# Performance work log

Hardware: AMD Instinct MI355X
Metric: run time of the kernel (lower is better)

Reference implementation:

```python
import jax, jax.numpy as jnp
import numpy as np

B, N, C, H = 4, 1025, 768, 12
KEEP_RATIO = 0.25
BETA = 1.0


def setup_inputs() -> dict:
    key = jax.random.key(0)
    k1, k2, k3, k4, k5 = jax.random.split(key, 5)
    x = jax.random.normal(k1, (B, N, C), dtype=jnp.float32)
    ucb_count_score = jax.random.uniform(k2, (H, N), dtype=jnp.float32)
    W_qkv = jax.random.normal(k3, (C, 3 * C), dtype=jnp.float32) * 0.02
    W_proj = jax.random.normal(k4, (C, C), dtype=jnp.float32) * 0.02
    b_proj = jax.random.normal(k5, (C,), dtype=jnp.float32) * 0.02
    return {"x": x, "ucb_count_score": ucb_count_score, "W_qkv": W_qkv,
            "W_proj": W_proj, "b_proj": b_proj, "counter": 100, "ucb_enabled": 1}


def reference(x, ucb_count_score, W_qkv, W_proj, b_proj, counter, ucb_enabled):
    Bn, Nn, Cn = x.shape
    Dh = Cn // H
    scale = Dh ** -0.5
    # qkv projection (no bias, qkv_bias=False)
    qkv = (x @ W_qkv).reshape(Bn, Nn, 3, H, Dh)
    q = jnp.transpose(qkv[:, :, 0], (0, 2, 1, 3))  # [B,H,N,Dh]
    k = jnp.transpose(qkv[:, :, 1], (0, 2, 1, 3))
    v = jnp.transpose(qkv[:, :, 2], (0, 2, 1, 3))
    attn_probs = jax.nn.softmax(jnp.einsum('bhnd,bhmd->bhnm', q, k) * scale, axis=-1)

    if ucb_enabled and counter > 50:
        # UCB pruning path (exclude_cls=True, keep_ratio set)
        total_patches = Nn - 1
        k_sel = max(1, int(total_patches * KEEP_RATIO))
        patch_scores = attn_probs[:, :, :, 1:].mean(axis=2)  # [B,H,N-1]
        expl = BETA * jnp.sqrt(jnp.log(counter + 1.0) / (ucb_count_score[:, 1:] + 1e-6))  # [H,N-1]
        global_ucb = (patch_scores + expl[None]).mean(axis=1)  # [B,N-1]
        _, sel = jax.lax.top_k(global_ucb, k_sel)  # [B,k]
        tok = sel + 1  # shift for CLS
        # keep[b,j] = 1 if token j is CLS or selected in batch b
        keep = jnp.zeros((Bn, Nn), dtype=attn_probs.dtype)
        keep = keep.at[jnp.arange(Bn)[:, None], tok].set(1.0).at[:, 0].set(1.0)
        # mask[b,h,i,j] = keep[b,i] OR keep[b,j]
        mask = jnp.maximum(keep[:, None, :, None], keep[:, None, None, :])
        pruned = attn_probs * mask
        pruned = pruned / (pruned.sum(axis=-1, keepdims=True) + 1e-8)
        context = jnp.einsum('bhnm,bhmd->bhnd', pruned, v)
        cnt = jnp.zeros((Nn,), dtype=jnp.float32).at[tok.reshape(-1)].add(1.0) / Bn
        score_delta = jnp.broadcast_to(cnt[None, :], ucb_count_score.shape)
    else:
        context = jnp.einsum('bhnm,bhmd->bhnd', attn_probs, v)
        score_delta = None

    out = context.transpose(0, 2, 1, 3).reshape(Bn, Nn, Cn) @ W_proj + b_proj
    return out, score_delta
```

## Files before the change

kernel.cpp:

```cpp
#include <hip/hip_runtime.h>
#include <hip/hip_bf16.h>
#include <math.h>

#define Bb 4
#define Nn 1025
#define Cc 768
#define Hh 12
#define BH (Bb*Hh)
#define M_ROWS 4100
#define KSEL 256
#define JP 1152
#define IT_TILES 68
#define NIB 17
#define NIB32 33
#define NSW 9
#define MT16 264
#define KC24 24
#define JT16 72
#define STR4 292
#define NPART 396
#define QSCALE 0.18033688011112042f

#define CAST_X_BLK 1584
#define CAST_WQKV_BLK 864
#define CAST_WPROJ_BLK 288

typedef __attribute__((ext_vector_type(8))) short short8;
typedef __attribute__((ext_vector_type(4))) short short4s;
typedef __attribute__((ext_vector_type(4))) float floatx4;

static __device__ inline unsigned short f2bf(float v) {
    __hip_bfloat16 b = __float2bfloat16(v);
    return *reinterpret_cast<unsigned short*>(&b);
}
static __device__ inline short tbfs(float f) {
    union { float f; unsigned u; } x; x.f = f;
    return (short)(x.u >> 16);
}
static __device__ inline float fexp2(float x) {
    return __builtin_amdgcn_exp2f(x);
}

static __device__ inline void async16(const unsigned short* g, unsigned short* l) {
    __builtin_amdgcn_global_load_lds(
        (const __attribute__((address_space(1))) unsigned int*)g,
        (__attribute__((address_space(3))) unsigned int*)l, 16, 0, 0);
}

__global__ __launch_bounds__(256)
void cast_all(const float* __restrict__ x, const float* __restrict__ Wqkv,
              const float* __restrict__ Wproj,
              unsigned short* __restrict__ xA, unsigned short* __restrict__ WB,
              unsigned short* __restrict__ WpB)
{
    int blk = blockIdx.x;
    int tid = threadIdx.x;
    if (blk < CAST_X_BLK) {
        int s = blk * 256 + tid;
        int ml = s & 15, q = (s >> 4) & 3;
        int t2 = s >> 6;
        int mt = t2 % MT16, kc = t2 / MT16;
        int m = mt * 16 + ml, k = kc * 32 + q * 8;
        uint4 pk = {0u, 0u, 0u, 0u};
        if (m < M_ROWS) {
            float4 a = *(const float4*)&x[(size_t)m * 768 + k];
            float4 b2 = *(const float4*)&x[(size_t)m * 768 + k + 4];
            pk.x = (unsigned)f2bf(a.x)  | ((unsigned)f2bf(a.y)  << 16);
            pk.y = (unsigned)f2bf(a.z)  | ((unsigned)f2bf(a.w)  << 16);
            pk.z = (unsigned)f2bf(b2.x) | ((unsigned)f2bf(b2.y) << 16);
            pk.w = (unsigned)f2bf(b2.z) | ((unsigned)f2bf(b2.w) << 16);
        }
        *(uint4*)&xA[(size_t)s * 8] = pk;
        return;
    }
    const float* W;
    unsigned short* WO;
    int N, NT, s;
    if (blk < CAST_X_BLK + CAST_WQKV_BLK) {
        W = Wqkv; WO = WB; N = 2304; NT = 144;
        s = (blk - CAST_X_BLK) * 256 + tid;
    } else {
        W = Wproj; WO = WpB; N = 768; NT = 48;
        s = (blk - CAST_X_BLK - CAST_WQKV_BLK) * 256 + tid;
    }
    int nl = s & 15, q = (s >> 4) & 3;
    int t2 = s >> 6;
    int nt = t2 % NT, kc = t2 / NT;
    int n = nt * 16 + nl, k = kc * 32 + q * 8;
    unsigned hv[8];
#pragma unroll
    for (int e = 0; e < 8; ++e)
        hv[e] = f2bf(W[(size_t)(k + e) * N + n]);
    uint4 pk;
    pk.x = hv[0] | (hv[1] << 16);
    pk.y = hv[2] | (hv[3] << 16);
    pk.z = hv[4] | (hv[5] << 16);
    pk.w = hv[6] | (hv[7] << 16);
    *(uint4*)&WO[(size_t)s * 8] = pk;
}

__global__ __launch_bounds__(256, 2)
void gemm_mfma(const unsigned short* __restrict__ Af,
               const unsigned short* __restrict__ Bf,
               int Nt16, int mode,
               unsigned short* __restrict__ qB, unsigned short* __restrict__ kF,
               unsigned short* __restrict__ vF,
               float* __restrict__ outp, const float* __restrict__ bias)
{
    __shared__ __align__(16) unsigned short ldsA[4096];
    __shared__ __align__(16) unsigned short ldsB[4096];
    const int tid = threadIdx.x;
    const int ln = tid & 63, w = tid >> 6;
    const int wm = w >> 1, wn = w & 1;
    const int mb = blockIdx.x, nb = blockIdx.y;

    floatx4 acc[4][4];
#pragma unroll
    for (int mt = 0; mt < 4; ++mt)
#pragma unroll
        for (int nt = 0; nt < 4; ++nt)
            acc[mt][nt] = (floatx4){0.f, 0.f, 0.f, 0.f};

    for (int kc = 0; kc < KC24; ++kc) {
        const unsigned short* gA = Af + ((size_t)(kc * MT16 + mb * 8)) * 512;
        const unsigned short* gB = Bf + ((size_t)(kc * Nt16 + nb * 8)) * 512;
        async16(gA + (size_t)(w * 128 + ln) * 8,      &ldsA[w * 1024]);
        async16(gA + (size_t)(w * 128 + 64 + ln) * 8, &ldsA[w * 1024 + 512]);
        async16(gB + (size_t)(w * 128 + ln) * 8,      &ldsB[w * 1024]);
        async16(gB + (size_t)(w * 128 + 64 + ln) * 8, &ldsB[w * 1024 + 512]);
        __syncthreads();

        short8 Am[4], Bn[4];
#pragma unroll
        for (int mt = 0; mt < 4; ++mt)
            Am[mt] = *(const short8*)&ldsA[((wm * 4 + mt) * 64 + ln) * 8];
#pragma unroll
        for (int nt = 0; nt < 4; ++nt)
            Bn[nt] = *(const short8*)&ldsB[((wn * 4 + nt) * 64 + ln) * 8];
#pragma unroll
        for (int mt = 0; mt < 4; ++mt)
#pragma unroll
            for (int nt = 0; nt < 4; ++nt)
                acc[mt][nt] = __builtin_amdgcn_mfma_f32_16x16x32_bf16(
                    Am[mt], Bn[nt], acc[mt][nt], 0, 0, 0);
        __syncthreads();
    }

    const int q = ln >> 4, l15 = ln & 15;
    if (mode == 1) {
#pragma unroll
        for (int nt = 0; nt < 4; ++nt) {
            int gn = nb * 128 + wn * 64 + nt * 16 + l15;
            float bv = bias[gn];
#pragma unroll
            for (int mt = 0; mt < 4; ++mt) {
                int gmb = mb * 128 + wm * 64 + mt * 16 + q * 4;
#pragma unroll
                for (int r = 0; r < 4; ++r) {
                    int gm = gmb + r;
                    if (gm < M_ROWS)
                        outp[(size_t)gm * 768 + gn] = acc[mt][nt][r] + bv;
                }
            }
        }
    } else {
#pragma unroll
        for (int nt = 0; nt < 4; ++nt) {
            int gn = nb * 128 + wn * 64 + nt * 16 + l15;
            int s = (gn >= 1536) ? 2 : (gn >= 768 ? 1 : 0);
            int rr = gn - s * Cc;
            int h = rr >> 6, d = rr & 63;
#pragma unroll
            for (int mt = 0; mt < 4; ++mt) {
                int gmb = mb * 128 + wm * 64 + mt * 16 + q * 4;
#pragma unroll
                for (int r = 0; r < 4; ++r) {
                    int gm = gmb + r;
                    if (gm >= M_ROWS) continue;
                    int b = gm / Nn;
                    int n = gm - b * Nn;
                    int bh = b * Hh + h;
                    float val = acc[mt][nt][r];
                    if (s == 0) {
                        int idx = (((bh * IT_TILES + (n >> 4)) * 2 + (d >> 5)) * 512)
                                  + ((((d & 31) >> 3) * 16 + (n & 15)) * 8) + (d & 7);
                        qB[idx] = f2bf(val * QSCALE);
                    } else if (s == 1) {
                        size_t idx = ((((size_t)bh * JT16 + (n >> 4)) * 2 + (d >> 5)) * 64
                                      + ((d >> 3) & 3) * 16 + (n & 15)) * 8 + (d & 7);
                        kF[idx] = f2bf(val);
                    } else {
                        size_t idx = ((((size_t)bh * JT16 + (n >> 4)) * 4 + (d >> 4)) * 64
                                      + ((n >> 2) & 3) * 16 + (d & 15)) * 4 + (n & 3);
                        vF[idx] = f2bf(val);
                    }
                }
            }
        }
    }
}

__global__ __launch_bounds__(256, 4)
void attn_colsum_mfma(const unsigned short* __restrict__ qB,
                      const unsigned short* __restrict__ kF,
                      float* __restrict__ colsum_part)
{
    __shared__ unsigned int expS8[32 * STR4];
    __shared__ float red16[16][32];
    __shared__ float linv[32];

    const int blk = blockIdx.x;
    const int x8 = blk & 7, g = blk >> 3;
    const int bh = x8 * 6 + (g % 6);
    const int ib = g / 6;
    const int tid = threadIdx.x;
    const int ws = tid >> 6;
    const int ln = tid & 63;
    const int i16 = ln & 15, q = ln >> 4;

    const unsigned short* kBase = kF + (size_t)bh * JT16 * 1024;

    short8 Qf[2][2];
#pragma unroll
    for (int it = 0; it < 2; ++it)
#pragma unroll
        for (int kc = 0; kc < 2; ++kc)
            Qf[it][kc] = *(const short8*)&qB[(((size_t)bh * IT_TILES + ib * 2 + it) * 2 + kc) * 512 + ln * 8];

    float lacc[2][2] = {{0.f, 0.f}, {0.f, 0.f}};

    short8 Kc[2][2], Kn[2][2];
#pragma unroll
    for (int jt = 0; jt < 2; ++jt)
#pragma unroll
        for (int kc = 0; kc < 2; ++kc)
            Kc[jt][kc] = *(const short8*)&kBase[(((ws * 2 + jt) * 2 + kc) * 64 + ln) * 8];

    for (int sw = 0; sw < NSW; ++sw) {
        if (sw + 1 < NSW) {
#pragma unroll
            for (int jt = 0; jt < 2; ++jt)
#pragma unroll
                for (int kc = 0; kc < 2; ++kc)
                    Kn[jt][kc] = *(const short8*)&kBase[((((sw + 1) * 8 + ws * 2 + jt) * 2 + kc) * 64 + ln) * 8];
        }

        floatx4 S[2][2];
#pragma unroll
        for (int it = 0; it < 2; ++it)
#pragma unroll
            for (int jt = 0; jt < 2; ++jt) {
                S[it][jt] = (floatx4){0.f, 0.f, 0.f, 0.f};
#pragma unroll
                for (int kc = 0; kc < 2; ++kc)
                    S[it][jt] = __builtin_amdgcn_mfma_f32_16x16x32_bf16(Kc[jt][kc], Qf[it][kc], S[it][jt], 0, 0, 0);
            }

        const int jbase0 = sw * 128 + ws * 32 + q * 4;
#pragma unroll
        for (int it = 0; it < 2; ++it) {
            const int irow = it * 16 + i16;
#pragma unroll
            for (int jt = 0; jt < 2; ++jt) {
                int jbase = jbase0 + jt * 16;
                float p[4];
#pragma unroll
                for (int r = 0; r < 4; ++r) {
                    float vld = (jbase + r < Nn) ? 1.f : 0.f;
                    p[r] = fexp2(S[it][jt][r]) * vld;
                }
                lacc[it][jt] += (p[0] + p[1]) + (p[2] + p[3]);
                unsigned u = (unsigned)__builtin_amdgcn_cvt_pk_fp8_f32(p[0], p[1], 0, false);
                u = (unsigned)__builtin_amdgcn_cvt_pk_fp8_f32(p[2], p[3], (int)u, true);
                expS8[irow * STR4 + (jbase >> 2)] = u;
            }
        }
#pragma unroll
        for (int jt = 0; jt < 2; ++jt)
#pragma unroll
            for (int kc = 0; kc < 2; ++kc)
                Kc[jt][kc] = Kn[jt][kc];
    }

    __syncthreads();
#pragma unroll
    for (int it = 0; it < 2; ++it)
        red16[ws * 4 + q][it * 16 + i16] = lacc[it][0] + lacc[it][1];
    __syncthreads();
    if (tid < 32) {
        float s = 0.f;
#pragma unroll
        for (int t = 0; t < 16; ++t) s += red16[t][tid];
        int gi = ib * 32 + tid;
        linv[tid] = (gi < Nn) ? 1.f / s : 0.f;
    }
    __syncthreads();

    float* prow = colsum_part + (size_t)(bh * NIB32 + ib) * JP;
    for (int grp = tid; grp < 288; grp += 256) {
        float a0 = 0.f, a1 = 0.f, a2 = 0.f, a3 = 0.f;
#pragma unroll 8
        for (int i = 0; i < 32; ++i) {
            unsigned v = expS8[i * STR4 + grp];
            float li = linv[i];
            a0 += __builtin_amdgcn_cvt_f32_fp8(v, 0) * li;
            a1 += __builtin_amdgcn_cvt_f32_fp8(v, 1) * li;
            a2 += __builtin_amdgcn_cvt_f32_fp8(v, 2) * li;
            a3 += __builtin_amdgcn_cvt_f32_fp8(v, 3) * li;
        }
        float4 o = {a0, a1, a2, a3};
        *(float4*)&prow[grp * 4] = o;
    }
}

__global__ __launch_bounds__(1024)
void ucb_topk(const float* __restrict__ colsum_part, const float* __restrict__ ucb_score,
              const int* __restrict__ counter_p,
              float* __restrict__ keepP, float* __restrict__ cnt_b)
{
    const int b = blockIdx.x;
    const int tid = threadIdx.x;
    __shared__ float vals[1024];
    __shared__ int   idxs[1024];

    for (int t = tid; t < JP; t += 1024) {
        keepP[b * JP + t] = 0.f;
        cnt_b[b * JP + t] = 0.f;
    }

    const int j = tid + 1;
    const float* pb = colsum_part + (size_t)b * NPART * JP + j;
    float c0 = 0.f, c1 = 0.f, c2 = 0.f, c3 = 0.f;
#pragma unroll 4
    for (int g2 = 0; g2 < NPART; g2 += 4) {
        c0 += pb[(size_t)(g2 + 0) * JP];
        c1 += pb[(size_t)(g2 + 1) * JP];
        c2 += pb[(size_t)(g2 + 2) * JP];
        c3 += pb[(size_t)(g2 + 3) * JP];
    }
    float cs = (c0 + c1) + (c2 + c3);

    float lc = logf((float)(*counter_p) + 1.0f);
    float s = cs * (1.0f / (float)Nn);
#pragma unroll
    for (int h = 0; h < Hh; ++h)
        s += sqrtf(lc / (ucb_score[h * Nn + j] + 1e-6f));
    s *= (1.0f / (float)Hh);
    vals[tid] = s; idxs[tid] = tid;
    __syncthreads();

    for (int k = 2; k <= 1024; k <<= 1) {
        for (int jj = k >> 1; jj > 0; jj >>= 1) {
            int partner = tid ^ jj;
            if (partner > tid) {
                float v1 = vals[tid], v2 = vals[partner];
                int i1 = idxs[tid], i2 = idxs[partner];
                bool gt = (v1 > v2) || (v1 == v2 && i1 < i2);
                bool desc = ((tid & k) == 0);
                if (desc ? !gt : gt) {
                    vals[tid] = v2; vals[partner] = v1;
                    idxs[tid] = i2; idxs[partner] = i1;
                }
            }
            __syncthreads();
        }
    }

    if (tid < KSEL) {
        int tok = idxs[tid] + 1;
        keepP[b * JP + tok] = 1.f;
        cnt_b[b * JP + tok] = 1.0f / (float)Bb;
    }
    if (tid == 0) keepP[b * JP + 0] = 1.f;
}

__global__ __launch_bounds__(256, 2)
void attn_ctx_mfma(const unsigned short* __restrict__ qB,
                   const unsigned short* __restrict__ kF,
                   const unsigned short* __restrict__ vF,
                   const float* __restrict__ keepP, const float* __restrict__ cnt_b,
                   unsigned short* __restrict__ ctxA, float* __restrict__ out2)
{
    __shared__ __align__(16) char smem[25856];
    float* keeps = (float*)smem;
    float* red16 = (float*)(smem + 4608);
    float* dinv  = (float*)(smem + 8704);
    float* redC  = (float*)(smem + 8960);

    const int blk = blockIdx.x;
    const int x8 = blk & 7, g = blk >> 3;
    const int bh = x8 * 6 + (g % 6);
    const int ib = g / 6;
    const int b = bh / Hh, h = bh % Hh;
    const int tid = threadIdx.x;
    const int ws = tid >> 6;
    const int ln = tid & 63;
    const int i16 = ln & 15, q = ln >> 4;

    {
        int t = blk * 256 + tid;
        if (t < Hh * Nn) {
            int n = t % Nn;
            out2[t] = cnt_b[0 * JP + n] + cnt_b[1 * JP + n]
                    + cnt_b[2 * JP + n] + cnt_b[3 * JP + n];
        }
    }

    for (int t = tid; t < JP; t += 256) keeps[t] = keepP[b * JP + t];

    const unsigned short* kBase = kF + (size_t)bh * JT16 * 1024;
    const unsigned short* vBase = vF + (size_t)bh * JT16 * 1024;

    short8 Qf[4][2];
#pragma unroll
    for (int it = 0; it < 4; ++it)
#pragma unroll
        for (int kc = 0; kc < 2; ++kc)
            Qf[it][kc] = *(const short8*)&qB[(((size_t)bh * IT_TILES + ib * 4 + it) * 2 + kc) * 512 + ln * 8];

    __syncthreads();

    float keepi[4];
#pragma unroll
    for (int it = 0; it < 4; ++it)
        keepi[it] = keeps[(ib * 4 + it) * 16 + i16];

    floatx4 ctxacc[4][4];
#pragma unroll
    for (int it = 0; it < 4; ++it)
#pragma unroll
        for (int dt = 0; dt < 4; ++dt)
            ctxacc[it][dt] = (floatx4){0.f, 0.f, 0.f, 0.f};
    float dsacc[4] = {0.f, 0.f, 0.f, 0.f};

    short8 Kc[2][2], Kn[2][2];
    short4s Vc[2][4], Vn[2][4];
#pragma unroll
    for (int jt = 0; jt < 2; ++jt) {
#pragma unroll
        for (int kc = 0; kc < 2; ++kc)
            Kc[jt][kc] = *(const short8*)&kBase[(((ws * 2 + jt) * 2 + kc) * 64 + ln) * 8];
#pragma unroll
        for (int dt = 0; dt < 4; ++dt)
            Vc[jt][dt] = *(const short4s*)&vBase[(((ws * 2 + jt) * 4 + dt) * 64 + ln) * 4];
    }

    for (int sw = 0; sw < NSW; ++sw) {
        if (sw + 1 < NSW) {
#pragma unroll
            for (int jt = 0; jt < 2; ++jt) {
#pragma unroll
                for (int kc = 0; kc < 2; ++kc)
                    Kn[jt][kc] = *(const short8*)&kBase[((((sw + 1) * 8 + ws * 2 + jt) * 2 + kc) * 64 + ln) * 8];
#pragma unroll
                for (int dt = 0; dt < 4; ++dt)
                    Vn[jt][dt] = *(const short4s*)&vBase[((((sw + 1) * 8 + ws * 2 + jt) * 4 + dt) * 64 + ln) * 4];
            }
        }

        float kjv[2][4], vld[2][4];
#pragma unroll
        for (int jt = 0; jt < 2; ++jt)
#pragma unroll
            for (int r = 0; r < 4; ++r) {
                int jj = sw * 128 + ws * 32 + jt * 16 + q * 4 + r;
                vld[jt][r] = (jj < Nn) ? 1.f : 0.f;
                kjv[jt][r] = keeps[jj];
            }

#pragma unroll
        for (int it = 0; it < 4; ++it) {
            floatx4 S[2];
#pragma unroll
            for (int jt = 0; jt < 2; ++jt) {
                S[jt] = (floatx4){0.f, 0.f, 0.f, 0.f};
#pragma unroll
                for (int kc = 0; kc < 2; ++kc)
                    S[jt] = __builtin_amdgcn_mfma_f32_16x16x32_bf16(Kc[jt][kc], Qf[it][kc], S[jt], 0, 0, 0);
            }
            bool rk = keepi[it] > 0.5f;
#pragma unroll
            for (int jt = 0; jt < 2; ++jt) {
                float p[4];
#pragma unroll
                for (int r = 0; r < 4; ++r) {
                    float w = rk ? vld[jt][r] : kjv[jt][r];
                    p[r] = fexp2(S[jt][r]) * w;
                    dsacc[it] += p[r];
                }
                short4s Pa;
                Pa.x = tbfs(p[0]); Pa.y = tbfs(p[1]);
                Pa.z = tbfs(p[2]); Pa.w = tbfs(p[3]);
#pragma unroll
                for (int dt = 0; dt < 4; ++dt)
                    ctxacc[it][dt] = __builtin_amdgcn_mfma_f32_16x16x16bf16_1k(
                        Pa, Vc[jt][dt], ctxacc[it][dt], 0, 0, 0);
            }
        }

#pragma unroll
        for (int jt = 0; jt < 2; ++jt) {
#pragma unroll
            for (int kc = 0; kc < 2; ++kc)
                Kc[jt][kc] = Kn[jt][kc];
#pragma unroll
            for (int dt = 0; dt < 4; ++dt)
                Vc[jt][dt] = Vn[jt][dt];
        }
    }

    __syncthreads();
#pragma unroll
    for (int it = 0; it < 4; ++it) red16[(ws * 4 + q) * 64 + it * 16 + i16] = dsacc[it];
    __syncthreads();
    if (tid < 64) {
        float s = 0.f;
#pragma unroll
        for (int t = 0; t < 16; ++t) s += red16[t * 64 + tid];
        dinv[tid] = 1.f / (s + 1e-8f);
    }
    for (int w = 0; w < 4; ++w) {
        __syncthreads();
        if (ws == w) {
#pragma unroll
            for (int it = 0; it < 4; ++it)
#pragma unroll
                for (int dt = 0; dt < 4; ++dt)
#pragma unroll
                    for (int r = 0; r < 4; ++r) {
                        int i = it * 16 + q * 4 + r;
                        int d = dt * 16 + i16;
                        float v = ctxacc[it][dt][r];
                        redC[i * 66 + d] = (w == 0) ? v : (redC[i * 66 + d] + v);
                    }
        }
    }
    __syncthreads();
#pragma unroll
    for (int rep = 0; rep < 2; ++rep) {
        int s2 = tid + rep * 256;
        int i = s2 >> 3, dc = s2 & 7;
        int gi = ib * 64 + i;
        if (gi < Nn) {
            int m = b * Nn + gi;
            float dv = dinv[i];
            const float* src = &redC[i * 66 + dc * 8];
            uint4 pk;
            pk.x = (unsigned)f2bf(src[0] * dv) | ((unsigned)f2bf(src[1] * dv) << 16);
            pk.y = (unsigned)f2bf(src[2] * dv) | ((unsigned)f2bf(src[3] * dv) << 16);
            pk.z = (unsigned)f2bf(src[4] * dv) | ((unsigned)f2bf(src[5] * dv) << 16);
            pk.w = (unsigned)f2bf(src[6] * dv) | ((unsigned)f2bf(src[7] * dv) << 16);
            int kc2 = h * 2 + (dc >> 2);
            int q2 = dc & 3;
            size_t idx = (((size_t)(kc2 * MT16 + (m >> 4))) * 64 + q2 * 16 + (m & 15)) * 8;
            *(uint4*)&ctxA[idx] = pk;
        }
    }
}

extern "C" void kernel_launch(void* const* d_in, const int* in_sizes, int n_in,
                              void* d_out, int out_size, void* d_ws, size_t ws_size,
                              hipStream_t stream) {
    const float* x     = (const float*)d_in[0];
    const float* ucb   = (const float*)d_in[1];
    const float* Wqkv  = (const float*)d_in[2];
    const float* Wproj = (const float*)d_in[3];
    const float* bproj = (const float*)d_in[4];
    const int*   counter = (const int*)d_in[5];

    unsigned short* qB = (unsigned short*)d_ws;
    unsigned short* kF = qB + 3342336;
    unsigned short* vF = kF + 3538944;
    float* keepP    = (float*)(vF + 3538944);
    float* cnt_b    = keepP + 4608;
    unsigned short* ctxA = (unsigned short*)(cnt_b + 4608);
    unsigned short* xA   = ctxA + 3244032;
    unsigned short* WB   = xA + 3244032;
    unsigned short* WpB  = WB + 1769472;
    float* colsum_part = (float*)(WpB + 589824);

    float* out  = (float*)d_out;
    float* out2 = out + 3148800;

    cast_all<<<dim3(CAST_X_BLK + CAST_WQKV_BLK + CAST_WPROJ_BLK), dim3(256), 0, stream>>>(
        x, Wqkv, Wproj, xA, WB, WpB);
    gemm_mfma<<<dim3(33, 18), dim3(256), 0, stream>>>(
        xA, WB, 144, 0, qB, kF, vF, nullptr, nullptr);
    attn_colsum_mfma<<<dim3(8 * 198), dim3(256), 0, stream>>>(qB, kF, colsum_part);
    ucb_topk<<<dim3(Bb), dim3(1024), 0, stream>>>(colsum_part, ucb, counter, keepP, cnt_b);
    attn_ctx_mfma<<<dim3(8 * 102), dim3(256), 0, stream>>>(qB, kF, vF, keepP, cnt_b, ctxA, out2);
    gemm_mfma<<<dim3(33, 6), dim3(256), 0, stream>>>(
        ctxA, WpB, 48, 1, nullptr, nullptr, nullptr, out, bproj);
}
```

Measured before the change: 224.7 us.

## Split colsum reduction into parallel kernel and replace bitonic sort with radix-select top-k

```diff
diff --git a/kernel.cpp b/kernel.cpp
--- a/kernel.cpp
+++ b/kernel.cpp
@@ -19,6 +19,7 @@
 #define JT16 72
 #define STR4 292
 #define NPART 396
+#define NSCORE 1024
 #define QSCALE 0.18033688011112042f
 
 #define CAST_X_BLK 1584
@@ -313,61 +314,113 @@
     }
 }
 
+__global__ __launch_bounds__(256)
+void colsum_reduce(const float* __restrict__ colsum_part,
+                   const float* __restrict__ ucb_score,
+                   const int* __restrict__ counter_p,
+                   float* __restrict__ scoreF)
+{
+    const int b = blockIdx.x, jc = blockIdx.y;
+    const int tid = threadIdx.x;
+    const int j32 = tid & 31, grp = tid >> 5;
+    const int t = jc * 32 + j32 + 1;
+    __shared__ float red[8][32];
+
+    const float* pb = colsum_part + (size_t)b * NPART * JP + t;
+    float a0 = 0.f, a1 = 0.f;
+    int r = grp;
+    for (; r + 8 < NPART; r += 16) {
+        a0 += pb[(size_t)r * JP];
+        a1 += pb[(size_t)(r + 8) * JP];
+    }
+    for (; r < NPART; r += 8) a0 += pb[(size_t)r * JP];
+    red[grp][j32] = a0 + a1;
+    __syncthreads();
+
+    if (tid < 32) {
+        float cs = 0.f;
+#pragma unroll
+        for (int g = 0; g < 8; ++g) cs += red[g][tid];
+        int tt = jc * 32 + tid + 1;
+        float lc = logf((float)(*counter_p) + 1.0f);
+        float s = cs * (1.0f / (float)Nn);
+#pragma unroll
+        for (int h = 0; h < Hh; ++h)
+            s += sqrtf(lc / (ucb_score[h * Nn + tt] + 1e-6f));
+        s *= (1.0f / (float)Hh);
+        scoreF[b * NSCORE + tt - 1] = s;
+    }
+}
+
 __global__ __launch_bounds__(1024)
-void ucb_topk(const float* __restrict__ colsum_part, const float* __restrict__ ucb_score,
-              const int* __restrict__ counter_p,
+void ucb_topk(const float* __restrict__ scoreF,
               float* __restrict__ keepP, float* __restrict__ cnt_b)
 {
     const int b = blockIdx.x;
     const int tid = threadIdx.x;
-    __shared__ float vals[1024];
-    __shared__ int   idxs[1024];
-
-    for (int t = tid; t < JP; t += 1024) {
-        keepP[b * JP + t] = 0.f;
-        cnt_b[b * JP + t] = 0.f;
-    }
-
-    const int j = tid + 1;
-    const float* pb = colsum_part + (size_t)b * NPART * JP + j;
-    float c0 = 0.f, c1 = 0.f, c2 = 0.f, c3 = 0.f;
-#pragma unroll 4
-    for (int g2 = 0; g2 < NPART; g2 += 4) {
-        c0 += pb[(size_t)(g2 + 0) * JP];
-        c1 += pb[(size_t)(g2 + 1) * JP];
-        c2 += pb[(size_t)(g2 + 2) * JP];
-        c3 += pb[(size_t)(g2 + 3) * JP];
-    }
-    float cs = (c0 + c1) + (c2 + c3);
-
-    float lc = logf((float)(*counter_p) + 1.0f);
-    float s = cs * (1.0f / (float)Nn);
-#pragma unroll
-    for (int h = 0; h < Hh; ++h)
-        s += sqrtf(lc / (ucb_score[h * Nn + j] + 1e-6f));
-    s *= (1.0f / (float)Hh);
-    vals[tid] = s; idxs[tid] = tid;
-    __syncthreads();
-
-    for (int k = 2; k <= 1024; k <<= 1) {
-        for (int jj = k >> 1; jj > 0; jj >>= 1) {
-            int partner = tid ^ jj;
-            if (partner > tid) {
-                float v1 = vals[tid], v2 = vals[partner];
-                int i1 = idxs[tid], i2 = idxs[partner];
-                bool gt = (v1 > v2) || (v1 == v2 && i1 < i2);
-                bool desc = ((tid & k) == 0);
-                if (desc ? !gt : gt) {
-                    vals[tid] = v2; vals[partner] = v1;
-                    idxs[tid] = i2; idxs[partner] = i1;
-                }
-            }
-            __syncthreads();
-        }
-    }
-
-    if (tid < KSEL) {
-        int tok = idxs[tid] + 1;
+    const int w = tid >> 6, ln = tid & 63;
+    __shared__ int hist[8192];
+    __shared__ int wtot[16];
+    __shared__ unsigned ckey[1024];
+    __shared__ int cidx[1024];
+    __shared__ int s_tb, s_rem, ccount;
+
+    for (int tpos = tid; tpos < JP; tpos += 1024) {
+        keepP[b * JP + tpos] = 0.f;
+        cnt_b[b * JP + tpos] = 0.f;
+    }
+
+    const unsigned key = __float_as_uint(scoreF[b * NSCORE + tid]);
+
+    for (int tpos = tid; tpos < 8192; tpos += 1024) hist[tpos] = 0;
+    if (tid == 0) ccount = 0;
+    __syncthreads();
+    atomicAdd(&hist[key >> 18], 1);
+    __syncthreads();
+
+    int part = 0;
+#pragma unroll
+    for (int q2 = 0; q2 < 8; ++q2) part += hist[tid * 8 + q2];
+    int v = part;
+#pragma unroll
+    for (int off = 1; off < 64; off <<= 1) {
+        int tv = __shfl_down(v, off);
+        if (ln + off < 64) v += tv;
+    }
+    if (ln == 0) wtot[w] = v;
+    __syncthreads();
+    int woff = 0;
+    for (int w2 = w + 1; w2 < 16; ++w2) woff += wtot[w2];
+    int cum_above = v + woff - part;
+    for (int q2 = 7; q2 >= 0; --q2) {
+        int c = hist[tid * 8 + q2];
+        if (cum_above < KSEL && cum_above + c >= KSEL) {
+            s_tb = tid * 8 + q2;
+            s_rem = KSEL - cum_above;
+        }
+        cum_above += c;
+    }
+    __syncthreads();
+
+    const int tb = s_tb, rem = s_rem;
+    const int mybin = (int)(key >> 18);
+    bool sel = mybin > tb;
+    if (mybin == tb) {
+        int p = atomicAdd(&ccount, 1);
+        ckey[p] = key; cidx[p] = tid;
+    }
+    __syncthreads();
+    if (mybin == tb) {
+        int rr = 0;
+        const int cc = ccount;
+        for (int c = 0; c < cc; ++c) {
+            unsigned kc2 = ckey[c]; int ic = cidx[c];
+            if (kc2 > key || (kc2 == key && ic < tid)) ++rr;
+        }
+        sel = rr < rem;
+    }
+    if (sel) {
+        int tok = tid + 1;
         keepP[b * JP + tok] = 1.f;
         cnt_b[b * JP + tok] = 1.0f / (float)Bb;
     }
@@ -578,6 +631,7 @@
     unsigned short* WB   = xA + 3244032;
     unsigned short* WpB  = WB + 1769472;
     float* colsum_part = (float*)(WpB + 589824);
+    float* scoreF = colsum_part + 1824768;
 
     float* out  = (float*)d_out;
     float* out2 = out + 3148800;
@@ -587,7 +641,8 @@
     gemm_mfma<<<dim3(33, 18), dim3(256), 0, stream>>>(
         xA, WB, 144, 0, qB, kF, vF, nullptr, nullptr);
     attn_colsum_mfma<<<dim3(8 * 198), dim3(256), 0, stream>>>(qB, kF, colsum_part);
-    ucb_topk<<<dim3(Bb), dim3(1024), 0, stream>>>(colsum_part, ucb, counter, keepP, cnt_b);
+    colsum_reduce<<<dim3(Bb, 32), dim3(256), 0, stream>>>(colsum_part, ucb, counter, scoreF);
+    ucb_topk<<<dim3(Bb), dim3(1024), 0, stream>>>(scoreF, keepP, cnt_b);
     attn_ctx_mfma<<<dim3(8 * 102), dim3(256), 0, stream>>>(qB, kF, vF, keepP, cnt_b, ctxA, out2);
     gemm_mfma<<<dim3(33, 6), dim3(256), 0, stream>>>(
         ctxA, WpB, 48, 1, nullptr, nullptr, nullptr, out, bproj);
```

New measurement: 206.2 us. 1.09x faster.
